# Kernel tuning notes

Measured on AMD Instinct MI355X. Metric: run time of the kernel, lower is better.

The kernel has to match this reference:

```python
import jax, jax.numpy as jnp
import numpy as np

N = 50000      # nodes
E = 800000     # edges (avg degree 16)
F_IN = 128     # num_features
HID = 128      # hidden_channels
C = 40         # num_classes


def setup_inputs() -> dict:
    key = jax.random.key(0)
    ks = jax.random.split(key, 8)
    x = jax.random.normal(ks[0], (N, F_IN), dtype=jnp.float32)
    edge_index = jax.random.randint(ks[1], (2, E), 0, N, dtype=jnp.int64)
    def glorot(k, fan_in, fan_out):
        s = np.sqrt(6.0 / (fan_in + fan_out)).astype(np.float32)
        return jax.random.uniform(k, (fan_in, fan_out), jnp.float32, -s, s)
    return {
        "x": x,
        "W1": glorot(ks[2], F_IN, HID), "b1": jnp.zeros((HID,), jnp.float32),
        "W2": glorot(ks[3], HID, HID),  "b2": jnp.zeros((HID,), jnp.float32),
        "W3": glorot(ks[4], HID, C),   "b3": jnp.zeros((C,), jnp.float32),
        "edge_index": edge_index,
    }


def reference(x, W1, b1, W2, b2, W3, b3, edge_index):
    # GCN with symmetric normalization and self-loops (PyG GCNConv semantics),
    # eval mode (dropout p=0.0), log-softmax output.
    src = edge_index[0]
    dst = edge_index[1]
    loop = jnp.arange(N, dtype=edge_index.dtype)
    src = jnp.concatenate([src, loop])      # [E+N]
    dst = jnp.concatenate([dst, loop])      # [E+N]
    ew = jnp.ones((E + N,), jnp.float32)    # edge_weight=None -> ones
    # deg[i] = sum of incoming edge weights at node i (aggregation index = dst/col)
    deg = jax.ops.segment_sum(ew, dst, num_segments=N)
    dinv = jnp.where(deg > 0, jax.lax.rsqrt(deg), 0.0)
    norm = dinv[src] * ew * dinv[dst]       # [E+N]

    def conv(h, W, b):
        # linear transform first (no bias), then gather->scale->scatter-add, then bias
        m = (h @ W)[src] * norm[:, None]                      # [E+N, out]
        return jax.ops.segment_sum(m, dst, num_segments=N) + b

    h = jax.nn.relu(conv(x, W1, b1))
    h = jax.nn.relu(conv(h, W2, b2))
    h = conv(h, W3, b3)
    return jax.nn.log_softmax(h, axis=-1)
```

## Files before the change

kernel.cpp:

```cpp
#include <hip/hip_runtime.h>
#include <math.h>

#define N_NODES 50000
#define N_EDGES 800000
#define BUCKET 64

typedef __attribute__((ext_vector_type(8))) short short8;
typedef __attribute__((ext_vector_type(4))) float f32x4;

__device__ __forceinline__ ushort f2bf(float f) {
    union { float f; uint u; } v; v.f = f;
    uint r = v.u + 0x7FFFu + ((v.u >> 16) & 1u);
    return (ushort)(r >> 16);
}
__device__ __forceinline__ float bflo(uint p) {
    union { uint u; float f; } v; v.u = p << 16; return v.f;
}
__device__ __forceinline__ float bfhi(uint p) {
    union { uint u; float f; } v; v.u = p & 0xFFFF0000u; return v.f;
}

__global__ void zero_cnt_k(int* __restrict__ cnt) {
    int i = blockIdx.x * 256 + threadIdx.x;
    if (i < N_NODES) cnt[i] = 0;
}

__global__ void scatter_k(const int* __restrict__ src, const int* __restrict__ dst,
                          int* __restrict__ cnt, int* __restrict__ colb) {
    int e = blockIdx.x * 256 + threadIdx.x;
    if (e < N_EDGES) {
        int d = dst[e];
        int pos = atomicAdd(&cnt[d], 1);
        colb[(size_t)d * BUCKET + pos] = src[e];
    }
}

__global__ void dinv_k(const int* __restrict__ cnt, float* __restrict__ dinv) {
    int i = blockIdx.x * 256 + threadIdx.x;
    if (i < N_NODES) dinv[i] = rsqrtf((float)(cnt[i] + 1));
}

template <int NT, bool CVT>
__global__ __launch_bounds__(512) void gemm_mfma_k(const void* __restrict__ Av,
                                                   const float* __restrict__ W,
                                                   ushort* __restrict__ Y,
                                                   const int fout) {
    __shared__ ushort sB[4 * NT * 64 * 8];
    const int tid = threadIdx.x;
    constexpr int FP = NT * 16;
    for (int i = tid; i < 128 * FP; i += 512) {
        const int k = i / FP, n = i % FP;
        const int s = k >> 5, r2 = (k >> 3) & 3, j = k & 7;
        const int t = n >> 4, nl = n & 15;
        const int l = r2 * 16 + nl;
        const int lp = (l & 56) | ((l + (l >> 3)) & 7);
        sB[(((s * NT + t) * 64) + lp) * 8 + j] = (n < fout) ? f2bf(W[k * fout + n]) : (ushort)0;
    }
    __syncthreads();

    const int wid = tid >> 6, lane = tid & 63;
    const int lp = (lane & 56) | ((lane + (lane >> 3)) & 7);
    const int t0 = blockIdx.x * 16 + wid * 2;
    const int t1 = t0 + 1;
    const int t0c = min(t0, N_NODES / 16 - 1);
    const int t1c = min(t1, N_NODES / 16 - 1);

    f32x4 acc[2][NT];
#pragma unroll
    for (int u = 0; u < 2; u++)
#pragma unroll
        for (int t = 0; t < NT; t++) acc[u][t] = (f32x4){0.f, 0.f, 0.f, 0.f};

#pragma unroll
    for (int s = 0; s < 4; s++) {
        short8 a0, a1;
        const int ko = 32 * s + 8 * (lane >> 4);
        if (CVT) {
            const float* Af = (const float*)Av;
            const float4* p0 = reinterpret_cast<const float4*>(Af + (size_t)(t0c * 16 + (lane & 15)) * 128 + ko);
            const float4* p1 = reinterpret_cast<const float4*>(Af + (size_t)(t1c * 16 + (lane & 15)) * 128 + ko);
            float4 u0 = p0[0], u1 = p0[1], v0 = p1[0], v1 = p1[1];
            a0[0] = f2bf(u0.x); a0[1] = f2bf(u0.y); a0[2] = f2bf(u0.z); a0[3] = f2bf(u0.w);
            a0[4] = f2bf(u1.x); a0[5] = f2bf(u1.y); a0[6] = f2bf(u1.z); a0[7] = f2bf(u1.w);
            a1[0] = f2bf(v0.x); a1[1] = f2bf(v0.y); a1[2] = f2bf(v0.z); a1[3] = f2bf(v0.w);
            a1[4] = f2bf(v1.x); a1[5] = f2bf(v1.y); a1[6] = f2bf(v1.z); a1[7] = f2bf(v1.w);
        } else {
            const ushort* Ab = (const ushort*)Av;
            a0 = *reinterpret_cast<const short8*>(Ab + (size_t)(t0c * 16 + (lane & 15)) * 128 + ko);
            a1 = *reinterpret_cast<const short8*>(Ab + (size_t)(t1c * 16 + (lane & 15)) * 128 + ko);
        }
#pragma unroll
        for (int t = 0; t < NT; t++) {
            short8 b = *reinterpret_cast<const short8*>(&sB[(((s * NT + t) * 64) + lp) * 8]);
            acc[0][t] = __builtin_amdgcn_mfma_f32_16x16x32_bf16(a0, b, acc[0][t], 0, 0, 0);
            acc[1][t] = __builtin_amdgcn_mfma_f32_16x16x32_bf16(a1, b, acc[1][t], 0, 0, 0);
        }
    }

    const int rl = 4 * (lane >> 4), cl = lane & 15;
#pragma unroll
    for (int u = 0; u < 2; u++) {
        const int tile = u ? t1 : t0;
        if (tile >= N_NODES / 16) continue;
        const int row0 = tile * 16;
#pragma unroll
        for (int t = 0; t < NT; t++) {
            const int c = 16 * t + cl;
            if (NT == 3 && c >= fout) continue;
#pragma unroll
            for (int g = 0; g < 4; g++)
                Y[(size_t)(row0 + rl + g) * fout + c] = f2bf(acc[u][t][g]);
        }
    }
}

template <bool RELU>
__global__ __launch_bounds__(256) void gather128_k(const ushort* __restrict__ XW,
                                                   const int* __restrict__ cnt,
                                                   const int* __restrict__ colb,
                                                   const float* __restrict__ dinv,
                                                   const float* __restrict__ bias,
                                                   ushort* __restrict__ out) {
    const int node = (blockIdx.x * 256 + threadIdx.x) >> 6;
    const int lane = threadIdx.x & 63;
    if (node >= N_NODES) return;
    const float di = dinv[node];
    const int n = cnt[node];
    const int4* bucket = reinterpret_cast<const int4*>(colb + (size_t)node * BUCKET);
    const uint* XW32 = reinterpret_cast<const uint*>(XW);

    float a0 = 0.f, a1 = 0.f, b0 = 0.f, b1 = 0.f;
    float c0 = 0.f, c1 = 0.f, d0 = 0.f, d1 = 0.f;
    int e = 0;
    for (; e + 4 <= n; e += 4) {
        const int4 s4 = bucket[e >> 2];
        const float w0 = dinv[s4.x] * di, w1 = dinv[s4.y] * di;
        const float w2 = dinv[s4.z] * di, w3 = dinv[s4.w] * di;
        const uint p0 = XW32[(size_t)s4.x * 64 + lane];
        const uint p1 = XW32[(size_t)s4.y * 64 + lane];
        const uint p2 = XW32[(size_t)s4.z * 64 + lane];
        const uint p3 = XW32[(size_t)s4.w * 64 + lane];
        a0 = fmaf(bflo(p0), w0, a0); a1 = fmaf(bfhi(p0), w0, a1);
        b0 = fmaf(bflo(p1), w1, b0); b1 = fmaf(bfhi(p1), w1, b1);
        c0 = fmaf(bflo(p2), w2, c0); c1 = fmaf(bfhi(p2), w2, c1);
        d0 = fmaf(bflo(p3), w3, d0); d1 = fmaf(bfhi(p3), w3, d1);
    }
    for (; e < n; e++) {
        const int s = colb[(size_t)node * BUCKET + e];
        const float w = dinv[s] * di;
        const uint p = XW32[(size_t)s * 64 + lane];
        a0 = fmaf(bflo(p), w, a0); a1 = fmaf(bfhi(p), w, a1);
    }
    const uint ps = XW32[(size_t)node * 64 + lane];
    const float ws = di * di;
    a0 = fmaf(bflo(ps), ws, (a0 + b0) + (c0 + d0)) + bias[2 * lane];
    a1 = fmaf(bfhi(ps), ws, (a1 + b1) + (c1 + d1)) + bias[2 * lane + 1];
    if (RELU) { a0 = fmaxf(a0, 0.f); a1 = fmaxf(a1, 0.f); }
    reinterpret_cast<uint*>(out)[(size_t)node * 64 + lane] =
        (uint)f2bf(a0) | ((uint)f2bf(a1) << 16);
}

__global__ __launch_bounds__(256) void gather40_lsm_k(const ushort* __restrict__ XW,
                                                      const int* __restrict__ cnt,
                                                      const int* __restrict__ colb,
                                                      const float* __restrict__ dinv,
                                                      const float* __restrict__ bias,
                                                      float* __restrict__ out) {
    const int node = (blockIdx.x * 256 + threadIdx.x) >> 6;
    const int lane = threadIdx.x & 63;
    if (node >= N_NODES) return;
    const int g = lane < 20 ? 0 : (lane < 40 ? 1 : 2);
    const int ll = lane - g * 20;
    const int llc = min(ll, 19);
    const float di = dinv[node];
    const int n = cnt[node];
    const uint* XW32 = reinterpret_cast<const uint*>(XW);

    float a0 = 0.f, a1 = 0.f;
    for (int e = g; e < n; e += 3) {
        const int s = colb[(size_t)node * BUCKET + e];
        const float w = dinv[s] * di;
        const uint p = XW32[(size_t)s * 20 + llc];
        a0 = fmaf(bflo(p), w, a0); a1 = fmaf(bfhi(p), w, a1);
    }
    const float t1 = __shfl(a0, lane + 20), t2 = __shfl(a0, lane + 40);
    const float u1 = __shfl(a1, lane + 20), u2 = __shfl(a1, lane + 40);
    float v0 = -INFINITY, v1 = -INFINITY;
    if (lane < 20) {
        const float s0 = a0 + t1 + t2, s1 = a1 + u1 + u2;
        const uint ps = XW32[(size_t)node * 20 + lane];
        const float ws = di * di;
        v0 = fmaf(bflo(ps), ws, s0) + bias[2 * lane];
        v1 = fmaf(bfhi(ps), ws, s1) + bias[2 * lane + 1];
    }
    float m = fmaxf(v0, v1);
#pragma unroll
    for (int o = 32; o > 0; o >>= 1) m = fmaxf(m, __shfl_xor(m, o));
    float s = (lane < 20) ? (expf(v0 - m) + expf(v1 - m)) : 0.f;
#pragma unroll
    for (int o = 32; o > 0; o >>= 1) s += __shfl_xor(s, o);
    if (lane < 20) {
        const float ls = m + logf(s);
        float2 r; r.x = v0 - ls; r.y = v1 - ls;
        reinterpret_cast<float2*>(out)[(size_t)node * 20 + lane] = r;
    }
}

extern "C" void kernel_launch(void* const* d_in, const int* in_sizes, int n_in,
                              void* d_out, int out_size, void* d_ws, size_t ws_size,
                              hipStream_t stream) {
    const float* x  = (const float*)d_in[0];
    const float* W1 = (const float*)d_in[1];
    const float* b1 = (const float*)d_in[2];
    const float* W2 = (const float*)d_in[3];
    const float* b2 = (const float*)d_in[4];
    const float* W3 = (const float*)d_in[5];
    const float* b3 = (const float*)d_in[6];
    const int* ei   = (const int*)d_in[7];
    const int* srcp = ei;
    const int* dstp = ei + N_EDGES;
    float* out = (float*)d_out;

    int*    cnt  = (int*)d_ws;
    float*  dinv = (float*)(cnt + 50176);
    int*    colb = (int*)(dinv + 50176);
    ushort* B0   = (ushort*)(colb + (size_t)N_NODES * BUCKET);
    ushort* B1   = B0 + (size_t)N_NODES * 128;

    const int NB_N = (N_NODES + 255) / 256;
    const int NB_E = (N_EDGES + 255) / 256;
    const int NB_W = (N_NODES * 64) / 256;
    const int NB_G = (N_NODES / 16 + 15) / 16;

    zero_cnt_k<<<NB_N, 256, 0, stream>>>(cnt);
    scatter_k<<<NB_E, 256, 0, stream>>>(srcp, dstp, cnt, colb);
    dinv_k<<<NB_N, 256, 0, stream>>>(cnt, dinv);

    gemm_mfma_k<8, true><<<NB_G, 512, 0, stream>>>(x, W1, B1, 128);
    gather128_k<true><<<NB_W, 256, 0, stream>>>(B1, cnt, colb, dinv, b1, B0);
    gemm_mfma_k<8, false><<<NB_G, 512, 0, stream>>>(B0, W2, B1, 128);
    gather128_k<true><<<NB_W, 256, 0, stream>>>(B1, cnt, colb, dinv, b2, B0);
    gemm_mfma_k<3, false><<<NB_G, 512, 0, stream>>>(B0, W3, B1, 40);
    gather40_lsm_k<<<NB_W, 256, 0, stream>>>(B1, cnt, colb, dinv, b3, out);
}
```

Baseline: 298.4 us.

## Fuse first-layer GEMM with edge bucketing scatter in one launch

Merges the independent first-layer x@W1 MFMA GEMM and the edge-to-bucket scatter into a single kernel. The first GEMM_BLKS blocks do the GEMM and the rest do the scatter, with each thread handling four edges through int4 loads. The zeroing kernel becomes a hipMemsetAsync, and the separate fp32 GEMM template path is dropped. The goal is fewer launches and overlapping the atomic-bound scatter with the compute-bound GEMM on different CUs, at the cost of a larger mixed-role kernel.

Result: faster. 275.2 us (-7.8%).

```diff
diff --git a/kernel.cpp b/kernel.cpp
--- a/kernel.cpp
+++ b/kernel.cpp
@@ -4,6 +4,8 @@
 #define N_NODES 50000
 #define N_EDGES 800000
 #define BUCKET 64
+#define GEMM_BLKS 196
+#define SCAT_BLKS 391
 
 typedef __attribute__((ext_vector_type(8))) short short8;
 typedef __attribute__((ext_vector_type(4))) float f32x4;
@@ -20,28 +22,96 @@
     union { uint u; float f; } v; v.u = p & 0xFFFF0000u; return v.f;
 }
 
-__global__ void zero_cnt_k(int* __restrict__ cnt) {
-    int i = blockIdx.x * 256 + threadIdx.x;
-    if (i < N_NODES) cnt[i] = 0;
-}
-
-__global__ void scatter_k(const int* __restrict__ src, const int* __restrict__ dst,
-                          int* __restrict__ cnt, int* __restrict__ colb) {
-    int e = blockIdx.x * 256 + threadIdx.x;
-    if (e < N_EDGES) {
-        int d = dst[e];
-        int pos = atomicAdd(&cnt[d], 1);
-        colb[(size_t)d * BUCKET + pos] = src[e];
-    }
-}
-
 __global__ void dinv_k(const int* __restrict__ cnt, float* __restrict__ dinv) {
     int i = blockIdx.x * 256 + threadIdx.x;
     if (i < N_NODES) dinv[i] = rsqrtf((float)(cnt[i] + 1));
 }
 
-template <int NT, bool CVT>
-__global__ __launch_bounds__(512) void gemm_mfma_k(const void* __restrict__ Av,
+__global__ __launch_bounds__(512) void fused_gemm1_scatter_k(
+        const float* __restrict__ Af, const float* __restrict__ W, ushort* __restrict__ Y,
+        const int* __restrict__ src, const int* __restrict__ dst,
+        int* __restrict__ cnt, int* __restrict__ colb) {
+    constexpr int NT = 8;
+    __shared__ ushort sB[4 * NT * 64 * 8];
+    const int tid = threadIdx.x;
+
+    if (blockIdx.x >= GEMM_BLKS) {
+        const int t = (blockIdx.x - GEMM_BLKS) * 512 + tid;
+        if (t >= N_EDGES / 4) return;
+        const int4 s4 = reinterpret_cast<const int4*>(src)[t];
+        const int4 d4 = reinterpret_cast<const int4*>(dst)[t];
+        int p0 = atomicAdd(&cnt[d4.x], 1);
+        int p1 = atomicAdd(&cnt[d4.y], 1);
+        int p2 = atomicAdd(&cnt[d4.z], 1);
+        int p3 = atomicAdd(&cnt[d4.w], 1);
+        colb[(size_t)d4.x * BUCKET + p0] = s4.x;
+        colb[(size_t)d4.y * BUCKET + p1] = s4.y;
+        colb[(size_t)d4.z * BUCKET + p2] = s4.z;
+        colb[(size_t)d4.w * BUCKET + p3] = s4.w;
+        return;
+    }
+
+    constexpr int FP = NT * 16;
+    for (int i = tid; i < 128 * FP; i += 512) {
+        const int k = i / FP, n = i % FP;
+        const int s = k >> 5, r2 = (k >> 3) & 3, j = k & 7;
+        const int t = n >> 4, nl = n & 15;
+        const int l = r2 * 16 + nl;
+        const int lp = (l & 56) | ((l + (l >> 3)) & 7);
+        sB[(((s * NT + t) * 64) + lp) * 8 + j] = f2bf(W[k * 128 + n]);
+    }
+    __syncthreads();
+
+    const int wid = tid >> 6, lane = tid & 63;
+    const int lp = (lane & 56) | ((lane + (lane >> 3)) & 7);
+    const int t0 = blockIdx.x * 16 + wid * 2;
+    const int t1 = t0 + 1;
+    const int t0c = min(t0, N_NODES / 16 - 1);
+    const int t1c = min(t1, N_NODES / 16 - 1);
+
+    f32x4 acc[2][NT];
+#pragma unroll
+    for (int u = 0; u < 2; u++)
+#pragma unroll
+        for (int t = 0; t < NT; t++) acc[u][t] = (f32x4){0.f, 0.f, 0.f, 0.f};
+
+#pragma unroll
+    for (int s = 0; s < 4; s++) {
+        short8 a0, a1;
+        const int ko = 32 * s + 8 * (lane >> 4);
+        const float4* p0 = reinterpret_cast<const float4*>(Af + (size_t)(t0c * 16 + (lane & 15)) * 128 + ko);
+        const float4* p1 = reinterpret_cast<const float4*>(Af + (size_t)(t1c * 16 + (lane & 15)) * 128 + ko);
+        float4 u0 = p0[0], u1 = p0[1], v0 = p1[0], v1 = p1[1];
+        a0[0] = f2bf(u0.x); a0[1] = f2bf(u0.y); a0[2] = f2bf(u0.z); a0[3] = f2bf(u0.w);
+        a0[4] = f2bf(u1.x); a0[5] = f2bf(u1.y); a0[6] = f2bf(u1.z); a0[7] = f2bf(u1.w);
+        a1[0] = f2bf(v0.x); a1[1] = f2bf(v0.y); a1[2] = f2bf(v0.z); a1[3] = f2bf(v0.w);
+        a1[4] = f2bf(v1.x); a1[5] = f2bf(v1.y); a1[6] = f2bf(v1.z); a1[7] = f2bf(v1.w);
+#pragma unroll
+        for (int t = 0; t < NT; t++) {
+            short8 b = *reinterpret_cast<const short8*>(&sB[(((s * NT + t) * 64) + lp) * 8]);
+            acc[0][t] = __builtin_amdgcn_mfma_f32_16x16x32_bf16(a0, b, acc[0][t], 0, 0, 0);
+            acc[1][t] = __builtin_amdgcn_mfma_f32_16x16x32_bf16(a1, b, acc[1][t], 0, 0, 0);
+        }
+    }
+
+    const int rl = 4 * (lane >> 4), cl = lane & 15;
+#pragma unroll
+    for (int u = 0; u < 2; u++) {
+        const int tile = u ? t1 : t0;
+        if (tile >= N_NODES / 16) continue;
+        const int row0 = tile * 16;
+#pragma unroll
+        for (int t = 0; t < NT; t++) {
+            const int c = 16 * t + cl;
+#pragma unroll
+            for (int g = 0; g < 4; g++)
+                Y[(size_t)(row0 + rl + g) * 128 + c] = f2bf(acc[u][t][g]);
+        }
+    }
+}
+
+template <int NT>
+__global__ __launch_bounds__(512) void gemm_mfma_k(const ushort* __restrict__ Ab,
                                                    const float* __restrict__ W,
                                                    ushort* __restrict__ Y,
                                                    const int fout) {
@@ -73,22 +143,9 @@
 
 #pragma unroll
     for (int s = 0; s < 4; s++) {
-        short8 a0, a1;
         const int ko = 32 * s + 8 * (lane >> 4);
-        if (CVT) {
-            const float* Af = (const float*)Av;
-            const float4* p0 = reinterpret_cast<const float4*>(Af + (size_t)(t0c * 16 + (lane & 15)) * 128 + ko);
-            const float4* p1 = reinterpret_cast<const float4*>(Af + (size_t)(t1c * 16 + (lane & 15)) * 128 + ko);
-            float4 u0 = p0[0], u1 = p0[1], v0 = p1[0], v1 = p1[1];
-            a0[0] = f2bf(u0.x); a0[1] = f2bf(u0.y); a0[2] = f2bf(u0.z); a0[3] = f2bf(u0.w);
-            a0[4] = f2bf(u1.x); a0[5] = f2bf(u1.y); a0[6] = f2bf(u1.z); a0[7] = f2bf(u1.w);
-            a1[0] = f2bf(v0.x); a1[1] = f2bf(v0.y); a1[2] = f2bf(v0.z); a1[3] = f2bf(v0.w);
-            a1[4] = f2bf(v1.x); a1[5] = f2bf(v1.y); a1[6] = f2bf(v1.z); a1[7] = f2bf(v1.w);
-        } else {
-            const ushort* Ab = (const ushort*)Av;
-            a0 = *reinterpret_cast<const short8*>(Ab + (size_t)(t0c * 16 + (lane & 15)) * 128 + ko);
-            a1 = *reinterpret_cast<const short8*>(Ab + (size_t)(t1c * 16 + (lane & 15)) * 128 + ko);
-        }
+        short8 a0 = *reinterpret_cast<const short8*>(Ab + (size_t)(t0c * 16 + (lane & 15)) * 128 + ko);
+        short8 a1 = *reinterpret_cast<const short8*>(Ab + (size_t)(t1c * 16 + (lane & 15)) * 128 + ko);
 #pragma unroll
         for (int t = 0; t < NT; t++) {
             short8 b = *reinterpret_cast<const short8*>(&sB[(((s * NT + t) * 64) + lp) * 8]);
@@ -228,18 +285,16 @@
     ushort* B1   = B0 + (size_t)N_NODES * 128;
 
     const int NB_N = (N_NODES + 255) / 256;
-    const int NB_E = (N_EDGES + 255) / 256;
     const int NB_W = (N_NODES * 64) / 256;
-    const int NB_G = (N_NODES / 16 + 15) / 16;
-
-    zero_cnt_k<<<NB_N, 256, 0, stream>>>(cnt);
-    scatter_k<<<NB_E, 256, 0, stream>>>(srcp, dstp, cnt, colb);
+
+    hipMemsetAsync(cnt, 0, 50176 * sizeof(int), stream);
+    fused_gemm1_scatter_k<<<GEMM_BLKS + SCAT_BLKS, 512, 0, stream>>>(
+        x, W1, B1, srcp, dstp, cnt, colb);
     dinv_k<<<NB_N, 256, 0, stream>>>(cnt, dinv);
 
-    gemm_mfma_k<8, true><<<NB_G, 512, 0, stream>>>(x, W1, B1, 128);
     gather128_k<true><<<NB_W, 256, 0, stream>>>(B1, cnt, colb, dinv, b1, B0);
-    gemm_mfma_k<8, false><<<NB_G, 512, 0, stream>>>(B0, W2, B1, 128);
+    gemm_mfma_k<8><<<GEMM_BLKS, 512, 0, stream>>>(B0, W2, B1, 128);
     gather128_k<true><<<NB_W, 256, 0, stream>>>(B1, cnt, colb, dinv, b2, B0);
-    gemm_mfma_k<3, false><<<NB_G, 512, 0, stream>>>(B0, W3, B1, 40);
+    gemm_mfma_k<3><<<GEMM_BLKS, 512, 0, stream>>>(B0, W3, B1, 40);
     gather40_lsm_k<<<NB_W, 256, 0, stream>>>(B1, cnt, colb, dinv, b3, out);
 }
```
